# Kernel optimization log

Measured on AMD Instinct MI355X. Metric: run time of the kernel, lower is better.

## Reference

```python
import jax, jax.numpy as jnp
import numpy as np

EPS = 1e-12


def conv3(x, W, b):
    # x: [B,C,H,W], W: [O,I,3,3] -> SAME conv, stride 1
    y = jax.lax.conv_general_dilated(x, W, (1, 1), 'SAME',
                                     dimension_numbers=('NCHW', 'OIHW', 'NCHW'))
    return y + b[None, :, None, None]


def unfold3(x):
    # torch F.unfold(kernel=3, padding=1): [B,C,H,W] -> [B, C*9, H*W]
    B, C, H, W = x.shape
    xp = jnp.pad(x, ((0, 0), (0, 0), (1, 1), (1, 1)))
    patches = jnp.stack([xp[:, :, i:i + H, j:j + W]
                         for i in range(3) for j in range(3)], axis=2)  # [B,C,9,H,W]
    return patches.reshape(B, C * 9, H * W)


def fold3(u, H, W):
    # torch F.fold(kernel=3, padding=1): [B, C*9, H*W] -> [B,C,H,W] (overlap-add)
    B = u.shape[0]
    C = u.shape[1] // 9
    p = u.reshape(B, C, 3, 3, H, W)
    out = jnp.zeros((B, C, H + 2, W + 2), u.dtype)
    for i in range(3):
        for j in range(3):
            out = out.at[:, :, i:i + H, j:j + W].add(p[:, :, i, j])
    return out[:, :, 1:-1, 1:-1]


def l2norm(v, axis):
    n = jnp.sqrt(jnp.sum(v * v, axis=axis, keepdims=True))
    return v / jnp.maximum(n, EPS)


def setup_inputs() -> dict:
    key = jax.random.key(0)
    ks = jax.random.split(key, 10)
    in_c, q_c = 64, 32
    B, H, W = 1, 96, 96
    s = 0.05
    return {
        'x':  jax.random.normal(ks[0], (B, in_c, H, W), jnp.float32),
        'W1': jax.random.normal(ks[1], (in_c, in_c, 3, 3), jnp.float32) * s,
        'b1': jax.random.normal(ks[2], (in_c,), jnp.float32) * s,
        'W2': jax.random.normal(ks[3], (in_c, in_c, 3, 3), jnp.float32) * s,
        'b2': jax.random.normal(ks[4], (in_c,), jnp.float32) * s,
        'Wq': jax.random.normal(ks[5], (q_c, in_c, 3, 3), jnp.float32) * s,
        'bq': jax.random.normal(ks[6], (q_c,), jnp.float32) * s,
        'Wk': jax.random.normal(ks[7], (q_c, in_c, 3, 3), jnp.float32) * s,
        'bk': jax.random.normal(ks[8], (q_c,), jnp.float32) * s,
    }


def reference(x, W1, b1, W2, b2, Wq, bq, Wk, bk):
    TOPK = 5
    B, C, H, W = x.shape
    L = H * W

    feature = jax.nn.relu(conv3(jax.nn.relu(conv3(x, W1, b1)), W2, b2))
    q = conv3(x, Wq, bq)
    k = conv3(x, Wk, bk)

    q_unfold = l2norm(unfold3(q), axis=1)                      # [B, Q9, L]
    k_unfold = l2norm(jnp.swapaxes(unfold3(k), 1, 2), axis=2)  # [B, L, Q9]

    R_qk = jnp.einsum('blc,bcm->blm', k_unfold, q_unfold)      # [B, L_k, L_q]

    # topk over dim=1 (key positions) for each query position
    vals, idxs = jax.lax.top_k(jnp.swapaxes(R_qk, 1, 2), TOPK)  # [B, L_q, K]
    R_maxs = jnp.swapaxes(vals, 1, 2)                           # [B, K, L]
    R_indexs = jnp.swapaxes(idxs, 1, 2)                         # [B, K, L]

    x_unfold = unfold3(x)                                       # [B, C*9, L]
    acc = jnp.zeros_like(x)
    for i in range(1, TOPK):
        idx = R_indexs[:, i, :][:, None, :]                     # [B,1,L]
        T_unfold = jnp.take_along_axis(x_unfold, idx, axis=2)   # [B, C*9, L]
        T = fold3(T_unfold, H, W) / 9.0
        S = R_maxs[:, i, :].reshape(B, 1, H, W)
        acc = acc + T * S
    y = feature + x + acc / float(TOPK - 1)
    return y
```

## Files before the change

kernel.cpp:

```cpp
#include <hip/hip_runtime.h>
#include <math.h>

#define HH 96
#define WW 96
#define LL 9216
#define PW 98
#define PCH (PW * PW)
#define D9 288
#define TOPK 5
#define NK 6
#define NCAND 8
#define KSPLIT 32
#define CPQ (KSPLIT * NK)
#define KEYS_PER_SPLIT (LL / KSPLIT)
#define PASSES (KEYS_PER_SPLIT / 32)
#define PCHUNK 1152

#define TOPK_BLOCKS 2304
#define CONV2_BLOCKS 576
#define TRANS_BLOCKS 144

typedef short short8 __attribute__((ext_vector_type(8)));
typedef float f32x16 __attribute__((ext_vector_type(16)));

__device__ __forceinline__ float  asf(unsigned u) { union { unsigned u; float f; } a; a.u = u; return a.f; }
__device__ __forceinline__ unsigned asu(float f)  { union { float f; unsigned u; } a; a.f = f; return a.u; }

__device__ __forceinline__ unsigned short f2bf(float f) {
    unsigned u = asu(f);
    unsigned r = u + 0x7fff + ((u >> 16) & 1);
    return (unsigned short)(r >> 16);
}

template<int N>
__device__ __forceinline__ void ins_med3(float* v, float x) {
    float nv[N];
    nv[0] = fmaxf(v[0], x);
    #pragma unroll
    for (int s = 1; s < N; ++s) nv[s] = __builtin_amdgcn_fmed3f(v[s-1], v[s], x);
    #pragma unroll
    for (int s = 0; s < N; ++s) v[s] = nv[s];
}

__device__ __forceinline__ bool better_tb(float av, int ai, float bv, int bi) {
    return (av > bv) || (av == bv && ai < bi);
}

template<int N>
__device__ __forceinline__ void insert_tb(float (&v)[N], int (&ix)[N], float nv, int ni) {
    if (better_tb(nv, ni, v[N-1], ix[N-1])) {
        v[N-1] = nv; ix[N-1] = ni;
        #pragma unroll
        for (int s = N-1; s > 0; --s) {
            if (better_tb(v[s], ix[s], v[s-1], ix[s-1])) {
                float tv = v[s]; v[s] = v[s-1]; v[s-1] = tv;
                int ti = ix[s]; ix[s] = ix[s-1]; ix[s-1] = ti;
            }
        }
    }
}

__global__ __launch_bounds__(256) void pad_init_kernel(
    const float* __restrict__ x, float* __restrict__ xpad, float* __restrict__ c1pad)
{
    int e = blockIdx.x * 256 + threadIdx.x;
    if (blockIdx.y == 1) { c1pad[e] = 0.0f; return; }
    int c = e / PCH, rem = e - c * PCH;
    int r = rem / PW, col = rem - r * PW;
    float val = 0.0f;
    if ((unsigned)(r - 1) < 96u && (unsigned)(col - 1) < 96u)
        val = x[(size_t)c * LL + (r - 1) * WW + (col - 1)];
    xpad[e] = val;
}

template<int NCO>
__device__ __forceinline__ void conv_pipe(
    const float* __restrict__ inpad, const float* __restrict__ Wt,
    const float* __restrict__ bias, int co0, int pix0,
    float (&acc)[NCO][2])
{
    int y = pix0 / WW, x0 = pix0 - y * WW;
    const float* base = inpad + y * PW + x0;

    #pragma unroll
    for (int j = 0; j < NCO; ++j) acc[j][0] = acc[j][1] = bias[co0 + j];

    float2 A[3][2], B[3][2];
    #pragma unroll
    for (int u = 0; u < 3; ++u) {
        A[u][0] = *(const float2*)(base + u * PW);
        A[u][1] = *(const float2*)(base + u * PW + 2);
    }

    #pragma unroll 1
    for (int ci = 0; ci < 64; ci += 2) {
        const float* nb = base + (size_t)(ci + 1) * PCH;
        #pragma unroll
        for (int u = 0; u < 3; ++u) {
            B[u][0] = *(const float2*)(nb + u * PW);
            B[u][1] = *(const float2*)(nb + u * PW + 2);
        }
        {
            const float* wb = Wt + ((size_t)co0 * 64 + ci) * 9;
            #pragma unroll
            for (int j = 0; j < NCO; ++j) {
                const float* wp = wb + (size_t)j * 64 * 9;
                #pragma unroll
                for (int u = 0; u < 3; ++u) {
                    float r0 = A[u][0].x, r1 = A[u][0].y, r2 = A[u][1].x, r3 = A[u][1].y;
                    float w0 = wp[u*3], w1 = wp[u*3+1], w2 = wp[u*3+2];
                    acc[j][0] = fmaf(r0, w0, acc[j][0]);
                    acc[j][1] = fmaf(r1, w0, acc[j][1]);
                    acc[j][0] = fmaf(r1, w1, acc[j][0]);
                    acc[j][1] = fmaf(r2, w1, acc[j][1]);
                    acc[j][0] = fmaf(r2, w2, acc[j][0]);
                    acc[j][1] = fmaf(r3, w2, acc[j][1]);
                }
            }
        }
        if (ci + 2 < 64) {
            const float* nb2 = base + (size_t)(ci + 2) * PCH;
            #pragma unroll
            for (int u = 0; u < 3; ++u) {
                A[u][0] = *(const float2*)(nb2 + u * PW);
                A[u][1] = *(const float2*)(nb2 + u * PW + 2);
            }
        }
        {
            const float* wb = Wt + ((size_t)co0 * 64 + (ci + 1)) * 9;
            #pragma unroll
            for (int j = 0; j < NCO; ++j) {
                const float* wp = wb + (size_t)j * 64 * 9;
                #pragma unroll
                for (int u = 0; u < 3; ++u) {
                    float r0 = B[u][0].x, r1 = B[u][0].y, r2 = B[u][1].x, r3 = B[u][1].y;
                    float w0 = wp[u*3], w1 = wp[u*3+1], w2 = wp[u*3+2];
                    acc[j][0] = fmaf(r0, w0, acc[j][0]);
                    acc[j][1] = fmaf(r1, w0, acc[j][1]);
                    acc[j][0] = fmaf(r1, w1, acc[j][0]);
                    acc[j][1] = fmaf(r2, w1, acc[j][1]);
                    acc[j][0] = fmaf(r2, w2, acc[j][0]);
                    acc[j][1] = fmaf(r3, w2, acc[j][1]);
                }
            }
        }
    }
}

__global__ __launch_bounds__(256) void conv_stage1_kernel(
    const float* __restrict__ xpad,
    const float* __restrict__ W1, const float* __restrict__ b1, float* __restrict__ c1pad,
    const float* __restrict__ Wq, const float* __restrict__ bq,
    const float* __restrict__ Wk, const float* __restrict__ bk,
    float* __restrict__ qq, float* __restrict__ kk)
{
    int g = blockIdx.y;
    int pix0 = (blockIdx.x * 256 + threadIdx.x) * 2;
    int y = pix0 / WW, x0 = pix0 - y * WW;

    if (g < 16) {
        float acc[4][2];
        conv_pipe<4>(xpad, W1, b1, g * 4, pix0, acc);
        #pragma unroll
        for (int j = 0; j < 4; ++j) {
            float* o = c1pad + (size_t)(g * 4 + j) * PCH + (y + 1) * PW + (x0 + 1);
            o[0] = fmaxf(acc[j][0], 0.0f);
            o[1] = fmaxf(acc[j][1], 0.0f);
        }
    } else if (g < 24) {
        float acc[4][2];
        conv_pipe<4>(xpad, Wq, bq, (g - 16) * 4, pix0, acc);
        #pragma unroll
        for (int j = 0; j < 4; ++j)
            *(float2*)(qq + (size_t)((g - 16) * 4 + j) * LL + pix0) = make_float2(acc[j][0], acc[j][1]);
    } else {
        float acc[4][2];
        conv_pipe<4>(xpad, Wk, bk, (g - 24) * 4, pix0, acc);
        #pragma unroll
        for (int j = 0; j < 4; ++j)
            *(float2*)(kk + (size_t)((g - 24) * 4 + j) * LL + pix0) = make_float2(acc[j][0], acc[j][1]);
    }
}

__global__ __launch_bounds__(256) void unfold_norm_kernel(
    const float* __restrict__ qq, float* __restrict__ q_f32, unsigned short* __restrict__ q_bf,
    const float* __restrict__ kk, float* __restrict__ k_f32, short8* __restrict__ kn_afrag)
{
    int isK = blockIdx.y;
    const float* in = isK ? kk : qq;
    float* o32 = isK ? k_f32 : q_f32;

    __shared__ float tile[3][32][34];
    __shared__ float inv_s[32];
    int tid = threadIdx.x;
    int l0 = blockIdx.x * 32;
    int y = l0 / WW, xb = l0 % WW;

    #pragma unroll
    for (int j = 0; j < 13; ++j) {
        int f = j * 256 + tid;
        if (f < 3 * 32 * 34) {
            int col = f % 34, cc = (f / 34) & 31, r = f / (34 * 32);
            int yy = y + r - 1, xv = xb + col - 1;
            float val = ((unsigned)yy < 96u && (unsigned)xv < 96u)
                        ? in[(size_t)cc * LL + yy * 96 + xv] : 0.0f;
            tile[r][cc][col] = val;
        }
    }
    __syncthreads();

    {
        int pxl = tid >> 3, sub = tid & 7;
        float ss = 0.0f;
        #pragma unroll
        for (int cc = 0; cc < 4; ++cc) {
            int c = sub * 4 + cc;
            #pragma unroll
            for (int u = 0; u < 3; ++u)
                #pragma unroll
                for (int v = 0; v < 3; ++v) {
                    float val = tile[u][c][pxl + v];
                    ss = fmaf(val, val, ss);
                }
        }
        ss += __shfl_xor(ss, 1);
        ss += __shfl_xor(ss, 2);
        ss += __shfl_xor(ss, 4);
        if (sub == 0) inv_s[pxl] = 1.0f / fmaxf(sqrtf(ss), 1e-12f);
    }
    __syncthreads();

    #pragma unroll 1
    for (int it = 0; it < 9; ++it) {
        int e = it * 256 + tid;
        int pxl = e / 72, dc = e - pxl * 72;
        int l = l0 + pxl;
        float inv = inv_s[pxl];
        float4 o; float* op = &o.x;
        #pragma unroll
        for (int i = 0; i < 4; ++i) {
            int d = dc * 4 + i;
            int c = d / 9, rm = d - c * 9;
            int u = rm / 3, v = rm - u * 3;
            op[i] = tile[u][c][pxl + v] * inv;
        }
        *(float4*)(o32 + (size_t)l * D9 + dc * 4) = o;
        if (!isK) {
            unsigned short b4[4];
            #pragma unroll
            for (int i = 0; i < 4; ++i) b4[i] = f2bf(op[i]);
            *(uint2*)(q_bf + (size_t)l * D9 + dc * 4) = *(uint2*)b4;
        }
    }

    if (isK) {
        #pragma unroll 1
        for (int it = 0; it < 5; ++it) {
            int e = it * 256 + tid;
            if (e < 1152) {
                int j = e >> 5, pxl = e & 31;
                int dg = j >> 1, half = j & 1;
                float inv = inv_s[pxl];
                unsigned short b8[8];
                #pragma unroll
                for (int i = 0; i < 8; ++i) {
                    int d = dg * 16 + half * 8 + i;
                    int c = d / 9, rm = d - c * 9;
                    int u = rm / 3, v = rm - u * 3;
                    b8[i] = f2bf(tile[u][c][pxl + v] * inv);
                }
                kn_afrag[(size_t)((blockIdx.x * 18 + dg) * 64 + half * 32 + pxl)] = *(short8*)b8;
            }
        }
    }
}

__device__ __forceinline__ void topk_body(
    int bx, int tid, const unsigned short* __restrict__ qn_bf,
    const uint4* __restrict__ kn_afrag, float* __restrict__ valsQ, uint4* ks)
{
    int lane = tid & 63;
    int col = lane & 31, khalf = lane >> 5;
    int qtile = bx >> 5;
    int split = bx & 31;
    int q0w = qtile * 128 + (tid >> 6) * 32;

    short8 qf[18];
    {
        const unsigned short* qrow = qn_bf + (size_t)(q0w + col) * D9 + khalf * 8;
        #pragma unroll
        for (int dg = 0; dg < 18; ++dg)
            qf[dg] = *(const short8*)(qrow + dg * 16);
    }

    float lv[NK];
    #pragma unroll
    for (int s = 0; s < NK; ++s) lv[s] = -INFINITY;

    const uint4* afr = kn_afrag + (size_t)split * (PASSES * PCHUNK);

    uint4 pre[5];
    #pragma unroll
    for (int c0 = 0; c0 < 5; ++c0) {
        int c = tid + c0 * 256;
        if (c < PCHUNK) pre[c0] = afr[c];
    }
    #pragma unroll
    for (int c0 = 0; c0 < 5; ++c0) {
        int c = tid + c0 * 256;
        if (c < PCHUNK) ks[c] = pre[c0];
    }
    __syncthreads();

    for (int p = 0; p < PASSES; ++p) {
        if (p + 1 < PASSES) {
            #pragma unroll
            for (int c0 = 0; c0 < 5; ++c0) {
                int c = tid + c0 * 256;
                if (c < PCHUNK) pre[c0] = afr[(size_t)(p + 1) * PCHUNK + c];
            }
        }

        f32x16 acc = {};
        const uint4* kb = ks + (p & 1) * PCHUNK + lane;
        #pragma unroll
        for (int dg = 0; dg < 18; ++dg) {
            uint4 t = kb[dg * 64];
            short8 af;
            *(uint4*)&af = t;
            acc = __builtin_amdgcn_mfma_f32_32x32x16_bf16(af, qf[dg], acc, 0, 0, 0);
        }

        int lbase = p * 32 + 4 * khalf;
        #pragma unroll
        for (int r = 0; r < 16; ++r) {
            unsigned lkey = (unsigned)(lbase + (r & 3) + 8 * (r >> 2));
            ins_med3<NK>(lv, asf((asu(acc[r]) & 0xFFFFFE00u) | lkey));
        }

        if (p + 1 < PASSES) {
            #pragma unroll
            for (int c0 = 0; c0 < 5; ++c0) {
                int c = tid + c0 * 256;
                if (c < PCHUNK) ks[((p + 1) & 1) * PCHUNK + c] = pre[c0];
            }
        }
        __syncthreads();
    }

    {
        float pv[NK];
        #pragma unroll
        for (int s = 0; s < NK; ++s) pv[s] = __shfl_xor(lv[s], 32);
        #pragma unroll
        for (int s = 0; s < NK; ++s) ins_med3<NK>(lv, pv[s]);
        if (lane < 32) {
            int q = q0w + col;
            float* vq = valsQ + (size_t)q * CPQ + split * NK;
            #pragma unroll
            for (int s = 0; s < NK; ++s) vq[s] = lv[s];
        }
    }
}

__global__ __launch_bounds__(256, 3) void fused_main_kernel(
    const unsigned short* __restrict__ qn_bf, const uint4* __restrict__ kn_afrag,
    float* __restrict__ valsQ,
    const float* __restrict__ c1pad, const float* __restrict__ W2,
    const float* __restrict__ b2, float* __restrict__ feat,
    const float* __restrict__ x, float* __restrict__ xT)
{
    __shared__ alignas(16) char smem[2 * PCHUNK * 16];
    int bx = blockIdx.x, tid = threadIdx.x;

    if (bx < TOPK_BLOCKS) {
        topk_body(bx, tid, qn_bf, kn_afrag, valsQ, (uint4*)smem);
    } else if (bx < TOPK_BLOCKS + CONV2_BLOCKS) {
        int idx = bx - TOPK_BLOCKS;
        int cx = idx % 18, cy = idx / 18;
        int pix0 = (cx * 256 + tid) * 2;
        float acc[2][2];
        conv_pipe<2>(c1pad, W2, b2, cy * 2, pix0, acc);
        #pragma unroll
        for (int j = 0; j < 2; ++j) {
            float2 o;
            o.x = fmaxf(acc[j][0], 0.0f);
            o.y = fmaxf(acc[j][1], 0.0f);
            *(float2*)(feat + (size_t)(cy * 2 + j) * LL + pix0) = o;
        }
    } else {
        int idx = bx - TOPK_BLOCKS - CONV2_BLOCKS;
        float (*t)[65] = (float (*)[65])smem;
        int pix0 = idx * 64;
        int lp = tid & 63, cg = tid >> 6;
        #pragma unroll
        for (int cc = 0; cc < 16; ++cc) {
            int c = cg * 16 + cc;
            t[c][lp] = x[(size_t)c * LL + pix0 + lp];
        }
        __syncthreads();
        #pragma unroll
        for (int pp = 0; pp < 16; ++pp) {
            int pl = cg * 16 + pp;
            xT[(size_t)(pix0 + pl) * 64 + lp] = t[lp][pl];
        }
    }
}

__global__ __launch_bounds__(256) void rerank_kernel(
    const float* __restrict__ valsQ,
    const float* __restrict__ qn_f32, const float* __restrict__ kn_f32,
    float* __restrict__ vals, int* __restrict__ idxs)
{
    int tid = threadIdx.x;
    int lane = tid & 63;
    int half = lane >> 5, l32 = lane & 31;
    int q = blockIdx.x * 8 + (tid >> 6) * 2 + half;

    const float* vq = valsQ + (size_t)q * CPQ + l32 * NK;
    float v[NK];
    #pragma unroll
    for (int s = 0; s < NK; ++s) v[s] = vq[s];

    int ckey[NCAND];
    #pragma unroll
    for (int it = 0; it < NCAND; ++it) {
        float cv = v[0];
        int cl = l32;
        #pragma unroll
        for (int st = 1; st < 32; st <<= 1) {
            float ov = __shfl_xor(cv, st);
            int ol = __shfl_xor(cl, st);
            if (ov > cv || (ov == cv && ol < cl)) { cv = ov; cl = ol; }
        }
        ckey[it] = cl * KEYS_PER_SPLIT + (int)(asu(cv) & 0x1FFu);
        if (cl == l32) {
            #pragma unroll
            for (int s = 0; s < NK-1; ++s) v[s] = v[s+1];
            v[NK-1] = -INFINITY;
        }
    }

    int r = l32 >> 2, part = l32 & 3;
    const float4* qr = (const float4*)(qn_f32 + (size_t)q * D9) + part * 18;
    const float4* kr = (const float4*)(kn_f32 + (size_t)ckey[r] * D9) + part * 18;
    float s0 = 0.f, s1 = 0.f, s2 = 0.f, s3 = 0.f;
    #pragma unroll
    for (int i2 = 0; i2 < 18; ++i2) {
        float4 a = qr[i2], b = kr[i2];
        s0 = fmaf(a.x, b.x, s0); s1 = fmaf(a.y, b.y, s1);
        s2 = fmaf(a.z, b.z, s2); s3 = fmaf(a.w, b.w, s3);
    }
    float sc = (s0 + s1) + (s2 + s3);
    sc += __shfl_xor(sc, 1);
    sc += __shfl_xor(sc, 2);

    float bv[TOPK]; int bi[TOPK];
    #pragma unroll
    for (int s = 0; s < TOPK; ++s) { bv[s] = -INFINITY; bi[s] = 0x7fffffff; }
    #pragma unroll
    for (int cc = 0; cc < NCAND; ++cc) {
        float sv = __shfl(sc, half * 32 + cc * 4);
        insert_tb<TOPK>(bv, bi, sv, ckey[cc]);
    }
    if (l32 == 0) {
        #pragma unroll
        for (int s = 0; s < TOPK; ++s) {
            vals[(size_t)s * LL + q] = bv[s];
            idxs[(size_t)s * LL + q] = bi[s];
        }
    }
}

__global__ __launch_bounds__(256) void gather_out_kernel(
    const float* __restrict__ xT, const float* __restrict__ feat,
    const float* __restrict__ vals, const int* __restrict__ idxs,
    float* __restrict__ out)
{
    int wave = threadIdx.x >> 6, lane = threadIdx.x & 63;
    int pix = blockIdx.x * 4 + wave;
    int y = pix / WW, x0 = pix - y * WW;
    float acc = 0.0f;
    #pragma unroll 1
    for (int s = 1; s < TOPK; ++s) {
        float S = vals[(size_t)s * LL + pix] * (1.0f/9.0f);
        #pragma unroll
        for (int i = 0; i < 3; ++i) {
            int qy = y + 1 - i;
            #pragma unroll
            for (int j = 0; j < 3; ++j) {
                int qx = x0 + 1 - j;
                if ((unsigned)qy < 96u && (unsigned)qx < 96u) {
                    int l = idxs[(size_t)s * LL + qy * WW + qx];
                    int yl = l / WW, xl = l - yl * WW;
                    int sy = yl + i - 1, sx = xl + j - 1;
                    if ((unsigned)sy < 96u && (unsigned)sx < 96u)
                        acc = fmaf(S, xT[(size_t)(sy * WW + sx) * 64 + lane], acc);
                }
            }
        }
    }
    out[(size_t)lane * LL + pix] = feat[(size_t)lane * LL + pix]
                                 + xT[(size_t)pix * 64 + lane] + acc * 0.25f;
}

extern "C" void kernel_launch(void* const* d_in, const int* in_sizes, int n_in,
                              void* d_out, int out_size, void* d_ws, size_t ws_size,
                              hipStream_t stream)
{
    (void)in_sizes; (void)n_in; (void)out_size; (void)ws_size;
    const float* x  = (const float*)d_in[0];
    const float* W1 = (const float*)d_in[1];
    const float* b1 = (const float*)d_in[2];
    const float* W2 = (const float*)d_in[3];
    const float* b2 = (const float*)d_in[4];
    const float* Wq = (const float*)d_in[5];
    const float* bq = (const float*)d_in[6];
    const float* Wk = (const float*)d_in[7];
    const float* bk = (const float*)d_in[8];
    float* out = (float*)d_out;

    char* p = (char*)d_ws;
    float* xpad   = (float*)p;            p += (size_t)64 * PCH * 4;
    float* c1pad  = (float*)p;            p += (size_t)64 * PCH * 4;
    float* feat   = (float*)p;            p += (size_t)64 * LL * 4;
    float* xT     = (float*)p;            p += (size_t)64 * LL * 4;
    float* qq     = (float*)p;            p += (size_t)32 * LL * 4;
    float* kk     = (float*)p;            p += (size_t)32 * LL * 4;
    float* qn_f32 = (float*)p;            p += (size_t)LL * D9 * 4;
    float* kn_f32 = (float*)p;            p += (size_t)LL * D9 * 4;
    unsigned short* qn_bf = (unsigned short*)p;  p += (size_t)LL * D9 * 2;
    short8* kn_afrag = (short8*)p;        p += (size_t)KSPLIT * PASSES * 18 * 64 * 16;
    float* valsQ  = (float*)p;            p += (size_t)LL * CPQ * 4;
    float* vals   = (float*)p;            p += (size_t)TOPK * LL * 4;
    int*   idxs   = (int*)p;              p += (size_t)TOPK * LL * 4;

    pad_init_kernel<<<dim3(2401, 2), 256, 0, stream>>>(x, xpad, c1pad);
    conv_stage1_kernel<<<dim3(18, 32), 256, 0, stream>>>(xpad, W1, b1, c1pad, Wq, bq, Wk, bk, qq, kk);
    unfold_norm_kernel<<<dim3(288, 2), 256, 0, stream>>>(qq, qn_f32, qn_bf, kk, kn_f32, kn_afrag);
    fused_main_kernel<<<TOPK_BLOCKS + CONV2_BLOCKS + TRANS_BLOCKS, 256, 0, stream>>>(
        qn_bf, (const uint4*)kn_afrag, valsQ, c1pad, W2, b2, feat, x, xT);
    rerank_kernel<<<LL / 8, 256, 0, stream>>>(valsQ, qn_f32, kn_f32, vals, idxs);
    gather_out_kernel<<<LL / 4, 256, 0, stream>>>(xT, feat, vals, idxs, out);
}
```

Before: 332.6 us.

## Unfuse top-k MFMA kernel and double query tile per warp for key reuse

Splits the fused top-k/conv2/transpose kernel back into three separate launches. The top-k kernel now has each wave process two 32-query tiles against the same LDS key fragment, issuing two MFMAs per key load. This halves the grid to 1152 blocks and the number of key-chunk loads per query. In exchange it doubles query-fragment and top-k register state (launch bound lowered to 2 blocks/CU), and conv2 and the transpose no longer overlap with the top-k work inside one launch.

Result: slower. 341.0 us (+2.5%).

```diff
diff --git a/kernel.cpp b/kernel.cpp
--- a/kernel.cpp
+++ b/kernel.cpp
@@ -16,10 +16,6 @@
 #define PASSES (KEYS_PER_SPLIT / 32)
 #define PCHUNK 1152
 
-#define TOPK_BLOCKS 2304
-#define CONV2_BLOCKS 576
-#define TRANS_BLOCKS 144
-
 typedef short short8 __attribute__((ext_vector_type(8)));
 typedef float f32x16 __attribute__((ext_vector_type(16)));
 
@@ -179,6 +175,41 @@
         #pragma unroll
         for (int j = 0; j < 4; ++j)
             *(float2*)(kk + (size_t)((g - 24) * 4 + j) * LL + pix0) = make_float2(acc[j][0], acc[j][1]);
+    }
+}
+
+__global__ __launch_bounds__(256) void conv2_kernel(
+    const float* __restrict__ c1pad, const float* __restrict__ W2,
+    const float* __restrict__ b2, float* __restrict__ feat)
+{
+    int pix0 = (blockIdx.x * 256 + threadIdx.x) * 2;
+    float acc[2][2];
+    conv_pipe<2>(c1pad, W2, b2, blockIdx.y * 2, pix0, acc);
+    #pragma unroll
+    for (int j = 0; j < 2; ++j) {
+        float2 o;
+        o.x = fmaxf(acc[j][0], 0.0f);
+        o.y = fmaxf(acc[j][1], 0.0f);
+        *(float2*)(feat + (size_t)(blockIdx.y * 2 + j) * LL + pix0) = o;
+    }
+}
+
+__global__ __launch_bounds__(256) void transpose_x_kernel(
+    const float* __restrict__ x, float* __restrict__ xT)
+{
+    __shared__ float t[64][65];
+    int pix0 = blockIdx.x * 64;
+    int lp = threadIdx.x & 63, cg = threadIdx.x >> 6;
+    #pragma unroll
+    for (int cc = 0; cc < 16; ++cc) {
+        int c = cg * 16 + cc;
+        t[c][lp] = x[(size_t)c * LL + pix0 + lp];
+    }
+    __syncthreads();
+    #pragma unroll
+    for (int pp = 0; pp < 16; ++pp) {
+        int pl = cg * 16 + pp;
+        xT[(size_t)(pix0 + pl) * 64 + lp] = t[lp][pl];
     }
 }
 
@@ -275,27 +306,31 @@
     }
 }
 
-__device__ __forceinline__ void topk_body(
-    int bx, int tid, const unsigned short* __restrict__ qn_bf,
-    const uint4* __restrict__ kn_afrag, float* __restrict__ valsQ, uint4* ks)
-{
+__global__ __launch_bounds__(256, 2) void topk_mfma_kernel(
+    const unsigned short* __restrict__ qn_bf, const uint4* __restrict__ kn_afrag,
+    float* __restrict__ valsQ)
+{
+    __shared__ alignas(16) uint4 ks[2][PCHUNK];
+
+    int tid = threadIdx.x;
     int lane = tid & 63;
     int col = lane & 31, khalf = lane >> 5;
-    int qtile = bx >> 5;
-    int split = bx & 31;
-    int q0w = qtile * 128 + (tid >> 6) * 32;
-
-    short8 qf[18];
-    {
-        const unsigned short* qrow = qn_bf + (size_t)(q0w + col) * D9 + khalf * 8;
+    int qtile = blockIdx.x >> 5;
+    int split = blockIdx.x & 31;
+    int q0w = qtile * 256 + (tid >> 6) * 64;
+
+    short8 qf[2][18];
+    #pragma unroll
+    for (int b = 0; b < 2; ++b) {
+        const unsigned short* qrow = qn_bf + (size_t)(q0w + b*32 + col) * D9 + khalf * 8;
         #pragma unroll
         for (int dg = 0; dg < 18; ++dg)
-            qf[dg] = *(const short8*)(qrow + dg * 16);
-    }
-
-    float lv[NK];
-    #pragma unroll
-    for (int s = 0; s < NK; ++s) lv[s] = -INFINITY;
+            qf[b][dg] = *(const short8*)(qrow + dg * 16);
+    }
+
+    float lv0[NK], lv1[NK];
+    #pragma unroll
+    for (int s = 0; s < NK; ++s) { lv0[s] = -INFINITY; lv1[s] = -INFINITY; }
 
     const uint4* afr = kn_afrag + (size_t)split * (PASSES * PCHUNK);
 
@@ -308,7 +343,7 @@
     #pragma unroll
     for (int c0 = 0; c0 < 5; ++c0) {
         int c = tid + c0 * 256;
-        if (c < PCHUNK) ks[c] = pre[c0];
+        if (c < PCHUNK) ks[0][c] = pre[c0];
     }
     __syncthreads();
 
@@ -321,88 +356,48 @@
             }
         }
 
-        f32x16 acc = {};
-        const uint4* kb = ks + (p & 1) * PCHUNK + lane;
+        f32x16 acc0 = {}, acc1 = {};
+        const uint4* kb = ks[p & 1] + lane;
         #pragma unroll
         for (int dg = 0; dg < 18; ++dg) {
             uint4 t = kb[dg * 64];
             short8 af;
             *(uint4*)&af = t;
-            acc = __builtin_amdgcn_mfma_f32_32x32x16_bf16(af, qf[dg], acc, 0, 0, 0);
+            acc0 = __builtin_amdgcn_mfma_f32_32x32x16_bf16(af, qf[0][dg], acc0, 0, 0, 0);
+            acc1 = __builtin_amdgcn_mfma_f32_32x32x16_bf16(af, qf[1][dg], acc1, 0, 0, 0);
         }
 
         int lbase = p * 32 + 4 * khalf;
         #pragma unroll
         for (int r = 0; r < 16; ++r) {
             unsigned lkey = (unsigned)(lbase + (r & 3) + 8 * (r >> 2));
-            ins_med3<NK>(lv, asf((asu(acc[r]) & 0xFFFFFE00u) | lkey));
+            ins_med3<NK>(lv0, asf((asu(acc0[r]) & 0xFFFFFE00u) | lkey));
+            ins_med3<NK>(lv1, asf((asu(acc1[r]) & 0xFFFFFE00u) | lkey));
         }
 
         if (p + 1 < PASSES) {
             #pragma unroll
             for (int c0 = 0; c0 < 5; ++c0) {
                 int c = tid + c0 * 256;
-                if (c < PCHUNK) ks[((p + 1) & 1) * PCHUNK + c] = pre[c0];
+                if (c < PCHUNK) ks[(p + 1) & 1][c] = pre[c0];
             }
         }
         __syncthreads();
     }
 
-    {
+    #pragma unroll
+    for (int b = 0; b < 2; ++b) {
+        float* lv = b ? lv1 : lv0;
         float pv[NK];
         #pragma unroll
         for (int s = 0; s < NK; ++s) pv[s] = __shfl_xor(lv[s], 32);
         #pragma unroll
         for (int s = 0; s < NK; ++s) ins_med3<NK>(lv, pv[s]);
         if (lane < 32) {
-            int q = q0w + col;
+            int q = q0w + b * 32 + col;
             float* vq = valsQ + (size_t)q * CPQ + split * NK;
             #pragma unroll
             for (int s = 0; s < NK; ++s) vq[s] = lv[s];
-        }
-    }
-}
-
-__global__ __launch_bounds__(256, 3) void fused_main_kernel(
-    const unsigned short* __restrict__ qn_bf, const uint4* __restrict__ kn_afrag,
-    float* __restrict__ valsQ,
-    const float* __restrict__ c1pad, const float* __restrict__ W2,
-    const float* __restrict__ b2, float* __restrict__ feat,
-    const float* __restrict__ x, float* __restrict__ xT)
-{
-    __shared__ alignas(16) char smem[2 * PCHUNK * 16];
-    int bx = blockIdx.x, tid = threadIdx.x;
-
-    if (bx < TOPK_BLOCKS) {
-        topk_body(bx, tid, qn_bf, kn_afrag, valsQ, (uint4*)smem);
-    } else if (bx < TOPK_BLOCKS + CONV2_BLOCKS) {
-        int idx = bx - TOPK_BLOCKS;
-        int cx = idx % 18, cy = idx / 18;
-        int pix0 = (cx * 256 + tid) * 2;
-        float acc[2][2];
-        conv_pipe<2>(c1pad, W2, b2, cy * 2, pix0, acc);
-        #pragma unroll
-        for (int j = 0; j < 2; ++j) {
-            float2 o;
-            o.x = fmaxf(acc[j][0], 0.0f);
-            o.y = fmaxf(acc[j][1], 0.0f);
-            *(float2*)(feat + (size_t)(cy * 2 + j) * LL + pix0) = o;
-        }
-    } else {
-        int idx = bx - TOPK_BLOCKS - CONV2_BLOCKS;
-        float (*t)[65] = (float (*)[65])smem;
-        int pix0 = idx * 64;
-        int lp = tid & 63, cg = tid >> 6;
-        #pragma unroll
-        for (int cc = 0; cc < 16; ++cc) {
-            int c = cg * 16 + cc;
-            t[c][lp] = x[(size_t)c * LL + pix0 + lp];
-        }
-        __syncthreads();
-        #pragma unroll
-        for (int pp = 0; pp < 16; ++pp) {
-            int pl = cg * 16 + pp;
-            xT[(size_t)(pix0 + pl) * 64 + lp] = t[lp][pl];
         }
     }
 }
@@ -538,8 +533,9 @@
     pad_init_kernel<<<dim3(2401, 2), 256, 0, stream>>>(x, xpad, c1pad);
     conv_stage1_kernel<<<dim3(18, 32), 256, 0, stream>>>(xpad, W1, b1, c1pad, Wq, bq, Wk, bk, qq, kk);
     unfold_norm_kernel<<<dim3(288, 2), 256, 0, stream>>>(qq, qn_f32, qn_bf, kk, kn_f32, kn_afrag);
-    fused_main_kernel<<<TOPK_BLOCKS + CONV2_BLOCKS + TRANS_BLOCKS, 256, 0, stream>>>(
-        qn_bf, (const uint4*)kn_afrag, valsQ, c1pad, W2, b2, feat, x, xT);
+    topk_mfma_kernel<<<36 * KSPLIT, 256, 0, stream>>>(qn_bf, (const uint4*)kn_afrag, valsQ);
+    conv2_kernel<<<dim3(18, 32), 256, 0, stream>>>(c1pad, W2, b2, feat);
+    transpose_x_kernel<<<144, 256, 0, stream>>>(x, xT);
     rerank_kernel<<<LL / 8, 256, 0, stream>>>(valsQ, qn_f32, kn_f32, vals, idxs);
     gather_out_kernel<<<LL / 4, 256, 0, stream>>>(xT, feat, vals, idxs, out);
 }
```
